# Optimization experiments

Hardware: AMD Instinct MI355X
Metric: run time of the kernel (lower is better)

## Reference

```python
import jax, jax.numpy as jnp
import numpy as np

NUM_GROUPS = 17
NUM_OCCLUDED = 10
TEMP = 0.1


def setup_inputs() -> dict:
    key = jax.random.key(0)
    k1, k2 = jax.random.split(key)
    B, N, D = 128, 577, 768
    x = jax.random.normal(k1, (B, N, D), dtype=jnp.float32)
    # xavier_uniform-like scale for (D, G) weight
    bound = float(np.sqrt(6.0 / (D + NUM_GROUPS)))
    group_weights = jax.random.uniform(k2, (D, NUM_GROUPS), dtype=jnp.float32, minval=-bound, maxval=bound)
    return {"x": x, "group_weights": group_weights}


def _l2_normalize(v):
    # matches F.normalize(dim=-1, eps=1e-12)
    return v / jnp.maximum(jnp.linalg.norm(v, axis=-1, keepdims=True), 1e-12)


def reference(x, group_weights):
    B, N, D = x.shape
    cls_token = x[:, 0, :]            # (B, D)
    patch_tokens = x[:, 1:, :]        # (B, P, D), P = N-1

    # cosine similarity of each patch with cls token
    sim = jnp.einsum('bpd,bd->bp', _l2_normalize(patch_tokens), _l2_normalize(cls_token))  # (B, P)

    # k least-similar patches are "occluded" -> zero them out
    _, occ_idx = jax.lax.top_k(-sim, NUM_OCCLUDED)  # (B, K)
    mask = jnp.ones_like(sim).at[jnp.arange(B)[:, None], occ_idx].set(0.0)  # (B, P)
    non_occ = patch_tokens * mask[..., None]  # (B, P, D)

    # attention-style group pooling; softmax over groups (dim=1)
    scores = jnp.einsum('dg,bpd->bgp', group_weights, non_occ) / TEMP  # (B, G, P)
    attn = jax.nn.softmax(scores, axis=1)
    group_features = jnp.einsum('bgp,bpd->bgd', attn, non_occ)  # (B, G, D)

    # pack [global_feat, group_feat_1..G] as (B, 1+G, D)
    feats = jnp.concatenate([cls_token[:, None, :], group_features], axis=1)
    return feats, attn
```

## Files before the change

kernel.cpp:

```cpp
#include <hip/hip_runtime.h>
#include <math.h>

#define B_ 128
#define NTOK 577
#define P_ 576
#define D_ 768
#define G_ 17
#define KOCC 10
#define INV_TEMP 10.0f
#define U17 (1.0f / 17.0f)
#define NCHUNK 9

#define OFF_WT 0
#define OFF_SIM (G_ * D_)
#define OFF_CLSINV (OFF_SIM + B_ * P_)
#define OFF_GFP (OFF_CLSINV + B_)
#define GFP_PART ((size_t)B_ * G_ * D_)

__global__ __launch_bounds__(256) void k0_cls(const float* __restrict__ x,
                                              const float* __restrict__ gw,
                                              float* __restrict__ feats,
                                              float* __restrict__ clsinv,
                                              float* __restrict__ wt,
                                              int zero_groups) {
    if (blockIdx.x >= B_) {
        int g = blockIdx.x - B_;
        for (int d = threadIdx.x; d < D_; d += 256)
            wt[g * D_ + d] = gw[d * G_ + g];
        return;
    }
    int b = blockIdx.x;
    const float* cls = x + (size_t)b * NTOK * D_;
    float* fb = feats + (size_t)b * 18 * D_;
    float ss = 0.f;
    for (int i = threadIdx.x; i < D_ / 4; i += 256) {
        float4 v = ((const float4*)cls)[i];
        ((float4*)fb)[i] = v;
        ss = fmaf(v.x, v.x, fmaf(v.y, v.y, fmaf(v.z, v.z, fmaf(v.w, v.w, ss))));
    }
    if (zero_groups) {
        float4 z = {0.f, 0.f, 0.f, 0.f};
        for (int i = threadIdx.x; i < G_ * D_ / 4; i += 256)
            ((float4*)(fb + D_))[i] = z;
    }
    #pragma unroll
    for (int off = 32; off; off >>= 1) ss += __shfl_xor(ss, off, 64);
    __shared__ float red[4];
    int wave = threadIdx.x >> 6, lane = threadIdx.x & 63;
    if (lane == 0) red[wave] = ss;
    __syncthreads();
    if (threadIdx.x == 0) {
        float t = red[0] + red[1] + red[2] + red[3];
        clsinv[b] = 1.0f / fmaxf(sqrtf(t), 1e-12f);
    }
}

__global__ __launch_bounds__(256) void k13_score_pv(const float* __restrict__ x,
                                                    const float* __restrict__ wt,
                                                    const float* __restrict__ clsinv,
                                                    float* __restrict__ sim,
                                                    float* __restrict__ attn,
                                                    float* __restrict__ gfp,
                                                    float* __restrict__ feats,
                                                    int use_part) {
    __shared__ __align__(16) float atile[19 * 68];
    int tid = threadIdx.x;
    int b = blockIdx.y, chunk = blockIdx.x;
    const float* clsrow = x + (size_t)b * NTOK * D_;

    int lane = tid & 63, wave = tid >> 6;
    int lr = lane & 15, row4 = lane >> 4;
    int pbase = wave * 16 + row4 * 4;
    const float* xp0 = x + ((size_t)(b * NTOK + 1 + chunk * 64 + pbase)) * D_ + lr * 4;
    const float* wp  = wt + lr * 4;
    const float* cp  = clsrow + lr * 4;

    float4 xv[4], xn[4];
    #pragma unroll
    for (int m = 0; m < 4; ++m) xv[m] = *(const float4*)(xp0 + (size_t)m * D_);
    #pragma unroll
    for (int m = 0; m < 4; ++m) xn[m] = xv[m];

    float s[19][4];
    #pragma unroll
    for (int i = 0; i < 19; ++i)
        #pragma unroll
        for (int m = 0; m < 4; ++m) s[i][m] = 0.f;

    for (int kc = 0; kc < 12; ++kc) {
        if (kc < 11) {
            #pragma unroll
            for (int m = 0; m < 4; ++m)
                xn[m] = *(const float4*)(xp0 + (kc + 1) * 64 + (size_t)m * D_);
        }
        const float* wk = wp + kc * 64;
        float4 cls4 = *(const float4*)(cp + kc * 64);
        #pragma unroll
        for (int g = 0; g < 17; ++g) {
            float4 w4 = *(const float4*)(wk + (size_t)g * D_);
            #pragma unroll
            for (int m = 0; m < 4; ++m)
                s[g][m] = fmaf(xv[m].x, w4.x, fmaf(xv[m].y, w4.y,
                          fmaf(xv[m].z, w4.z, fmaf(xv[m].w, w4.w, s[g][m]))));
        }
        #pragma unroll
        for (int m = 0; m < 4; ++m)
            s[17][m] = fmaf(xv[m].x, cls4.x, fmaf(xv[m].y, cls4.y,
                       fmaf(xv[m].z, cls4.z, fmaf(xv[m].w, cls4.w, s[17][m]))));
        #pragma unroll
        for (int m = 0; m < 4; ++m)
            s[18][m] = fmaf(xv[m].x, xv[m].x, fmaf(xv[m].y, xv[m].y,
                       fmaf(xv[m].z, xv[m].z, fmaf(xv[m].w, xv[m].w, s[18][m]))));
        #pragma unroll
        for (int m = 0; m < 4; ++m) xv[m] = xn[m];
    }

    #pragma unroll
    for (int off = 8; off >= 1; off >>= 1)
        #pragma unroll
        for (int i = 0; i < 19; ++i)
            #pragma unroll
            for (int m = 0; m < 4; ++m)
                s[i][m] += __shfl_xor(s[i][m], off, 16);

    #pragma unroll
    for (int g = 0; g < 19; ++g) {
        if (lr == ((g < 16) ? g : 15)) {
            float4 v = {s[g][0], s[g][1], s[g][2], s[g][3]};
            *(float4*)&atile[g * 68 + pbase] = v;
        }
    }
    __syncthreads();

    if (tid < 64) {
        int p = chunk * 64 + tid;
        float v[17];
        float mx = -3.0e38f;
        #pragma unroll
        for (int g = 0; g < 17; ++g) {
            v[g] = atile[g * 68 + tid];
            mx = fmaxf(mx, v[g]);
        }
        float tot = 0.f;
        #pragma unroll
        for (int g = 0; g < 17; ++g) {
            v[g] = __expf((v[g] - mx) * INV_TEMP);
            tot += v[g];
        }
        float inv = 1.0f / tot;
        float* ap = attn + ((size_t)b * G_) * P_ + p;
        #pragma unroll
        for (int g = 0; g < 17; ++g) {
            float av = v[g] * inv;
            ap[(size_t)g * P_] = av;
            atile[g * 68 + tid] = av;
        }
        float cd = atile[17 * 68 + tid];
        float sq = atile[18 * 68 + tid];
        sim[(size_t)b * P_ + p] = cd * clsinv[b] / fmaxf(sqrtf(sq), 1e-12f);
    }
    __syncthreads();

    if (tid >= 192) return;
    const float* xb = x + ((size_t)(b * NTOK) + 1 + chunk * 64) * D_ + tid * 4;
    float4 acc[G_];
    #pragma unroll
    for (int g = 0; g < G_; ++g) acc[g] = make_float4(0.f, 0.f, 0.f, 0.f);

    float4 c0 = *(const float4*)(xb + (size_t)0 * D_);
    float4 c1 = *(const float4*)(xb + (size_t)1 * D_);
    float4 c2 = *(const float4*)(xb + (size_t)2 * D_);
    float4 c3 = *(const float4*)(xb + (size_t)3 * D_);

    for (int pp = 0; pp < 64; pp += 4) {
        float4 n0 = c0, n1 = c1, n2 = c2, n3 = c3;
        if (pp + 4 < 64) {
            n0 = *(const float4*)(xb + (size_t)(pp + 4) * D_);
            n1 = *(const float4*)(xb + (size_t)(pp + 5) * D_);
            n2 = *(const float4*)(xb + (size_t)(pp + 6) * D_);
            n3 = *(const float4*)(xb + (size_t)(pp + 7) * D_);
        }
        #pragma unroll
        for (int g = 0; g < G_; ++g) {
            float4 a = *(const float4*)&atile[g * 68 + pp];
            acc[g].x = fmaf(a.x, c0.x, fmaf(a.y, c1.x, fmaf(a.z, c2.x, fmaf(a.w, c3.x, acc[g].x))));
            acc[g].y = fmaf(a.x, c0.y, fmaf(a.y, c1.y, fmaf(a.z, c2.y, fmaf(a.w, c3.y, acc[g].y))));
            acc[g].z = fmaf(a.x, c0.z, fmaf(a.y, c1.z, fmaf(a.z, c2.z, fmaf(a.w, c3.z, acc[g].z))));
            acc[g].w = fmaf(a.x, c0.w, fmaf(a.y, c1.w, fmaf(a.z, c2.w, fmaf(a.w, c3.w, acc[g].w))));
        }
        c0 = n0; c1 = n1; c2 = n2; c3 = n3;
    }

    if (use_part) {
        float* gb = gfp + ((size_t)(chunk * B_ + b) * G_) * D_ + tid * 4;
        #pragma unroll
        for (int g = 0; g < G_; ++g) *(float4*)(gb + (size_t)g * D_) = acc[g];
    } else {
        float* fb = feats + ((size_t)(b * 18) + 1) * D_ + tid * 4;
        #pragma unroll
        for (int g = 0; g < G_; ++g) {
            atomicAdd(fb + (size_t)g * D_ + 0, acc[g].x);
            atomicAdd(fb + (size_t)g * D_ + 1, acc[g].y);
            atomicAdd(fb + (size_t)g * D_ + 2, acc[g].z);
            atomicAdd(fb + (size_t)g * D_ + 3, acc[g].w);
        }
    }
}

__global__ __launch_bounds__(192) void k24_fin(const float* __restrict__ x,
                                               const float* __restrict__ sim,
                                               const float* __restrict__ gfp,
                                               float* __restrict__ attn,
                                               float* __restrict__ feats,
                                               int use_part) {
    __shared__ int s_occ[KOCC];
    __shared__ float s_a0[KOCC][G_];
    int b = blockIdx.x, tid = threadIdx.x;

    if (tid < 64) {
        int lane = tid;
        int base = lane * 9;
        float v[9];
        #pragma unroll
        for (int j = 0; j < 9; ++j) v[j] = sim[(size_t)b * P_ + base + j];
        for (int t = 0; t < KOCC; ++t) {
            float mv = 3.0e38f;
            int mi = 1 << 30;
            #pragma unroll
            for (int j = 0; j < 9; ++j) {
                if (v[j] < mv) { mv = v[j]; mi = base + j; }
            }
            #pragma unroll
            for (int off = 1; off < 64; off <<= 1) {
                float ov = __shfl_xor(mv, off, 64);
                int oi = __shfl_xor(mi, off, 64);
                if (ov < mv || (ov == mv && oi < mi)) { mv = ov; mi = oi; }
            }
            if (lane == 0) s_occ[t] = mi;
            int loc = mi - base;
            if (loc >= 0 && loc < 9) v[loc] = 3.0e38f;
        }
    }

    float4 acc[G_];
    float* fb = feats + ((size_t)(b * 18) + 1) * D_ + tid * 4;
    if (use_part) {
        #pragma unroll
        for (int g = 0; g < G_; ++g) acc[g] = make_float4(0.f, 0.f, 0.f, 0.f);
        for (int pc = 0; pc < NCHUNK; ++pc) {
            const float* gb = gfp + ((size_t)(pc * B_ + b) * G_) * D_ + tid * 4;
            #pragma unroll
            for (int g = 0; g < G_; ++g) {
                float4 v = *(const float4*)(gb + (size_t)g * D_);
                acc[g].x += v.x; acc[g].y += v.y; acc[g].z += v.z; acc[g].w += v.w;
            }
        }
    } else {
        #pragma unroll
        for (int g = 0; g < G_; ++g) acc[g] = *(const float4*)(fb + (size_t)g * D_);
    }
    __syncthreads();

    for (int i = tid; i < KOCC * G_; i += 192) {
        int t = i / G_, g = i - t * G_;
        size_t idx = ((size_t)b * G_ + g) * P_ + s_occ[t];
        s_a0[t][g] = attn[idx];
        attn[idx] = U17;
    }
    __syncthreads();

    #pragma unroll
    for (int t = 0; t < KOCC; ++t) {
        float4 xo = *(const float4*)(x + ((size_t)(b * NTOK) + 1 + s_occ[t]) * D_ + tid * 4);
        #pragma unroll
        for (int g = 0; g < G_; ++g) {
            float a0 = s_a0[t][g];
            acc[g].x = fmaf(-a0, xo.x, acc[g].x);
            acc[g].y = fmaf(-a0, xo.y, acc[g].y);
            acc[g].z = fmaf(-a0, xo.z, acc[g].z);
            acc[g].w = fmaf(-a0, xo.w, acc[g].w);
        }
    }
    #pragma unroll
    for (int g = 0; g < G_; ++g) *(float4*)(fb + (size_t)g * D_) = acc[g];
}

extern "C" void kernel_launch(void* const* d_in, const int* in_sizes, int n_in,
                              void* d_out, int out_size, void* d_ws, size_t ws_size,
                              hipStream_t stream) {
    const float* x  = (const float*)d_in[0];
    const float* gw = (const float*)d_in[1];
    float* feats = (float*)d_out;
    float* attn  = (float*)d_out + (size_t)B_ * 18 * D_;
    float* wt      = (float*)d_ws + OFF_WT;
    float* sim     = (float*)d_ws + OFF_SIM;
    float* clsinv  = (float*)d_ws + OFF_CLSINV;
    float* gfp     = (float*)d_ws + OFF_GFP;

    int use_part = (((size_t)OFF_GFP + (size_t)NCHUNK * GFP_PART) * sizeof(float) <= ws_size);

    k0_cls<<<B_ + G_, 256, 0, stream>>>(x, gw, feats, clsinv, wt, !use_part);
    k13_score_pv<<<dim3(NCHUNK, B_), 256, 0, stream>>>(x, wt, clsinv, sim, attn, gfp, feats, use_part);
    k24_fin<<<B_, 192, 0, stream>>>(x, sim, gfp, attn, feats, use_part);
}
```

Measured before the change: 412.8 us.

## Stage group weights in LDS and triple-buffer x loads in score kernel

Copies the whole 17x768 group weight matrix into shared memory at block start, so inner-loop weight reads come from LDS instead of global/L1. It also replaces the double buffer of x rows with a three-slot rotating buffer that prefetches two k-chunks ahead, and reuses the LDS buffer as the score tile after a barrier. The change adds about 52 KB of LDS per block and more live registers, and sets launch_bounds to 3 blocks per CU, which may limit occupancy.

Result: slower. 705.6 us (+70.9%).

```diff
diff --git a/kernel.cpp b/kernel.cpp
--- a/kernel.cpp
+++ b/kernel.cpp
@@ -55,31 +55,42 @@
     }
 }
 
-__global__ __launch_bounds__(256) void k13_score_pv(const float* __restrict__ x,
-                                                    const float* __restrict__ wt,
-                                                    const float* __restrict__ clsinv,
-                                                    float* __restrict__ sim,
-                                                    float* __restrict__ attn,
-                                                    float* __restrict__ gfp,
-                                                    float* __restrict__ feats,
-                                                    int use_part) {
-    __shared__ __align__(16) float atile[19 * 68];
+__global__ __launch_bounds__(256, 3) void k13_score_pv(const float* __restrict__ x,
+                                                       const float* __restrict__ wt,
+                                                       const float* __restrict__ clsinv,
+                                                       float* __restrict__ sim,
+                                                       float* __restrict__ attn,
+                                                       float* __restrict__ gfp,
+                                                       float* __restrict__ feats,
+                                                       int use_part) {
+    __shared__ __align__(16) float wlds[G_ * D_];
+    float* atile = wlds;
+
     int tid = threadIdx.x;
     int b = blockIdx.y, chunk = blockIdx.x;
     const float* clsrow = x + (size_t)b * NTOK * D_;
 
+    for (int i = tid; i < G_ * D_ / 4; i += 256)
+        ((float4*)wlds)[i] = ((const float4*)wt)[i];
+
     int lane = tid & 63, wave = tid >> 6;
     int lr = lane & 15, row4 = lane >> 4;
+    int lr4 = lr * 4;
     int pbase = wave * 16 + row4 * 4;
-    const float* xp0 = x + ((size_t)(b * NTOK + 1 + chunk * 64 + pbase)) * D_ + lr * 4;
-    const float* wp  = wt + lr * 4;
-    const float* cp  = clsrow + lr * 4;
-
-    float4 xv[4], xn[4];
-    #pragma unroll
-    for (int m = 0; m < 4; ++m) xv[m] = *(const float4*)(xp0 + (size_t)m * D_);
-    #pragma unroll
-    for (int m = 0; m < 4; ++m) xn[m] = xv[m];
+    const float* xp0 = x + ((size_t)(b * NTOK + 1 + chunk * 64 + pbase)) * D_ + lr4;
+    const float* cp  = clsrow + lr4;
+
+    float4 xA[4], xB[4], xC[4];
+    float4 cA, cB, cC;
+    #pragma unroll
+    for (int m = 0; m < 4; ++m) xA[m] = *(const float4*)(xp0 + 0 * 64 + (size_t)m * D_);
+    #pragma unroll
+    for (int m = 0; m < 4; ++m) xB[m] = *(const float4*)(xp0 + 1 * 64 + (size_t)m * D_);
+    cA = *(const float4*)(cp + 0 * 64);
+    cB = *(const float4*)(cp + 1 * 64);
+    #pragma unroll
+    for (int m = 0; m < 4; ++m) xC[m] = xA[m];
+    cC = cA;
 
     float s[19][4];
     #pragma unroll
@@ -87,33 +98,42 @@
         #pragma unroll
         for (int m = 0; m < 4; ++m) s[i][m] = 0.f;
 
-    for (int kc = 0; kc < 12; ++kc) {
-        if (kc < 11) {
-            #pragma unroll
-            for (int m = 0; m < 4; ++m)
-                xn[m] = *(const float4*)(xp0 + (kc + 1) * 64 + (size_t)m * D_);
-        }
-        const float* wk = wp + kc * 64;
-        float4 cls4 = *(const float4*)(cp + kc * 64);
-        #pragma unroll
-        for (int g = 0; g < 17; ++g) {
-            float4 w4 = *(const float4*)(wk + (size_t)g * D_);
-            #pragma unroll
-            for (int m = 0; m < 4; ++m)
-                s[g][m] = fmaf(xv[m].x, w4.x, fmaf(xv[m].y, w4.y,
-                          fmaf(xv[m].z, w4.z, fmaf(xv[m].w, w4.w, s[g][m]))));
-        }
-        #pragma unroll
-        for (int m = 0; m < 4; ++m)
-            s[17][m] = fmaf(xv[m].x, cls4.x, fmaf(xv[m].y, cls4.y,
-                       fmaf(xv[m].z, cls4.z, fmaf(xv[m].w, cls4.w, s[17][m]))));
-        #pragma unroll
-        for (int m = 0; m < 4; ++m)
-            s[18][m] = fmaf(xv[m].x, xv[m].x, fmaf(xv[m].y, xv[m].y,
-                       fmaf(xv[m].z, xv[m].z, fmaf(xv[m].w, xv[m].w, s[18][m]))));
-        #pragma unroll
-        for (int m = 0; m < 4; ++m) xv[m] = xn[m];
-    }
+    __syncthreads();
+
+#define SCORE_BODY(XV, CV, XP, CP2, kcur)                                              \
+    do {                                                                               \
+        int kpre = (kcur) + 2;                                                         \
+        if (kpre < 12) {                                                               \
+            _Pragma("unroll")                                                          \
+            for (int m = 0; m < 4; ++m)                                                \
+                XP[m] = *(const float4*)(xp0 + kpre * 64 + (size_t)m * D_);            \
+            CP2 = *(const float4*)(cp + kpre * 64);                                    \
+        }                                                                              \
+        const float* wk = wlds + (kcur) * 64 + lr4;                                    \
+        _Pragma("unroll")                                                              \
+        for (int g = 0; g < 17; ++g) {                                                 \
+            float4 w4 = *(const float4*)(wk + (size_t)g * D_);                         \
+            _Pragma("unroll")                                                          \
+            for (int m = 0; m < 4; ++m)                                                \
+                s[g][m] = fmaf(XV[m].x, w4.x, fmaf(XV[m].y, w4.y,                      \
+                          fmaf(XV[m].z, w4.z, fmaf(XV[m].w, w4.w, s[g][m]))));         \
+        }                                                                              \
+        _Pragma("unroll")                                                              \
+        for (int m = 0; m < 4; ++m)                                                    \
+            s[17][m] = fmaf(XV[m].x, CV.x, fmaf(XV[m].y, CV.y,                         \
+                       fmaf(XV[m].z, CV.z, fmaf(XV[m].w, CV.w, s[17][m]))));           \
+        _Pragma("unroll")                                                              \
+        for (int m = 0; m < 4; ++m)                                                    \
+            s[18][m] = fmaf(XV[m].x, XV[m].x, fmaf(XV[m].y, XV[m].y,                   \
+                       fmaf(XV[m].z, XV[m].z, fmaf(XV[m].w, XV[m].w, s[18][m]))));     \
+    } while (0)
+
+    for (int kc = 0; kc < 12; kc += 3) {
+        SCORE_BODY(xA, cA, xC, cC, kc);
+        SCORE_BODY(xB, cB, xA, cA, kc + 1);
+        SCORE_BODY(xC, cC, xB, cB, kc + 2);
+    }
+#undef SCORE_BODY
 
     #pragma unroll
     for (int off = 8; off >= 1; off >>= 1)
@@ -122,6 +142,8 @@
             #pragma unroll
             for (int m = 0; m < 4; ++m)
                 s[i][m] += __shfl_xor(s[i][m], off, 16);
+
+    __syncthreads();
 
     #pragma unroll
     for (int g = 0; g < 19; ++g) {
```

## Split fused score+PV kernel into separate score and PV kernels

Applied to the files above, without the earlier changes.

Splits the fused scoring/softmax/PV kernel into two kernels. The score kernel runs 512 threads with 2 rows per thread instead of 4, cutting register pressure and raising occupancy. The PV kernel reloads attention from global memory into shared memory. The trade is a second pass over x (about 227MB read again), an extra launch, and a global round trip for attn.

Result: slower. 451.8 us (+9.4%).

```diff
diff --git a/kernel.cpp b/kernel.cpp
--- a/kernel.cpp
+++ b/kernel.cpp
@@ -55,64 +55,57 @@
     }
 }
 
-__global__ __launch_bounds__(256) void k13_score_pv(const float* __restrict__ x,
-                                                    const float* __restrict__ wt,
-                                                    const float* __restrict__ clsinv,
-                                                    float* __restrict__ sim,
-                                                    float* __restrict__ attn,
-                                                    float* __restrict__ gfp,
-                                                    float* __restrict__ feats,
-                                                    int use_part) {
+__global__ __launch_bounds__(512) void k1_score(const float* __restrict__ x,
+                                                const float* __restrict__ wt,
+                                                const float* __restrict__ clsinv,
+                                                float* __restrict__ sim,
+                                                float* __restrict__ attn) {
     __shared__ __align__(16) float atile[19 * 68];
     int tid = threadIdx.x;
     int b = blockIdx.y, chunk = blockIdx.x;
     const float* clsrow = x + (size_t)b * NTOK * D_;
 
     int lane = tid & 63, wave = tid >> 6;
-    int lr = lane & 15, row4 = lane >> 4;
-    int pbase = wave * 16 + row4 * 4;
-    const float* xp0 = x + ((size_t)(b * NTOK + 1 + chunk * 64 + pbase)) * D_ + lr * 4;
-    const float* wp  = wt + lr * 4;
-    const float* cp  = clsrow + lr * 4;
-
-    float4 xv[4], xn[4];
-    #pragma unroll
-    for (int m = 0; m < 4; ++m) xv[m] = *(const float4*)(xp0 + (size_t)m * D_);
-    #pragma unroll
-    for (int m = 0; m < 4; ++m) xn[m] = xv[m];
-
-    float s[19][4];
-    #pragma unroll
-    for (int i = 0; i < 19; ++i)
-        #pragma unroll
-        for (int m = 0; m < 4; ++m) s[i][m] = 0.f;
+    int lr = lane & 15, rh = lane >> 4;
+    int lr4 = lr * 4;
+    int pbase = wave * 8 + rh * 2;
+    const float* xp0 = x + ((size_t)(b * NTOK + 1 + chunk * 64 + pbase)) * D_ + lr4;
+    const float* cp  = clsrow + lr4;
+
+    float4 xv[2], xn[2], cv, cn;
+    xv[0] = *(const float4*)(xp0);
+    xv[1] = *(const float4*)(xp0 + D_);
+    cv = *(const float4*)(cp);
+    xn[0] = xv[0]; xn[1] = xv[1]; cn = cv;
+
+    float s[19][2];
+    #pragma unroll
+    for (int i = 0; i < 19; ++i) { s[i][0] = 0.f; s[i][1] = 0.f; }
 
     for (int kc = 0; kc < 12; ++kc) {
         if (kc < 11) {
-            #pragma unroll
-            for (int m = 0; m < 4; ++m)
-                xn[m] = *(const float4*)(xp0 + (kc + 1) * 64 + (size_t)m * D_);
-        }
-        const float* wk = wp + kc * 64;
-        float4 cls4 = *(const float4*)(cp + kc * 64);
+            xn[0] = *(const float4*)(xp0 + (kc + 1) * 64);
+            xn[1] = *(const float4*)(xp0 + (kc + 1) * 64 + D_);
+            cn = *(const float4*)(cp + (kc + 1) * 64);
+        }
+        const float* wk = wt + kc * 64 + lr4;
         #pragma unroll
         for (int g = 0; g < 17; ++g) {
             float4 w4 = *(const float4*)(wk + (size_t)g * D_);
             #pragma unroll
-            for (int m = 0; m < 4; ++m)
+            for (int m = 0; m < 2; ++m)
                 s[g][m] = fmaf(xv[m].x, w4.x, fmaf(xv[m].y, w4.y,
                           fmaf(xv[m].z, w4.z, fmaf(xv[m].w, w4.w, s[g][m]))));
         }
         #pragma unroll
-        for (int m = 0; m < 4; ++m)
-            s[17][m] = fmaf(xv[m].x, cls4.x, fmaf(xv[m].y, cls4.y,
-                       fmaf(xv[m].z, cls4.z, fmaf(xv[m].w, cls4.w, s[17][m]))));
-        #pragma unroll
-        for (int m = 0; m < 4; ++m)
+        for (int m = 0; m < 2; ++m)
+            s[17][m] = fmaf(xv[m].x, cv.x, fmaf(xv[m].y, cv.y,
+                       fmaf(xv[m].z, cv.z, fmaf(xv[m].w, cv.w, s[17][m]))));
+        #pragma unroll
+        for (int m = 0; m < 2; ++m)
             s[18][m] = fmaf(xv[m].x, xv[m].x, fmaf(xv[m].y, xv[m].y,
                        fmaf(xv[m].z, xv[m].z, fmaf(xv[m].w, xv[m].w, s[18][m]))));
-        #pragma unroll
-        for (int m = 0; m < 4; ++m) xv[m] = xn[m];
+        xv[0] = xn[0]; xv[1] = xn[1]; cv = cn;
     }
 
     #pragma unroll
@@ -120,14 +113,14 @@
         #pragma unroll
         for (int i = 0; i < 19; ++i)
             #pragma unroll
-            for (int m = 0; m < 4; ++m)
+            for (int m = 0; m < 2; ++m)
                 s[i][m] += __shfl_xor(s[i][m], off, 16);
 
     #pragma unroll
     for (int g = 0; g < 19; ++g) {
         if (lr == ((g < 16) ? g : 15)) {
-            float4 v = {s[g][0], s[g][1], s[g][2], s[g][3]};
-            *(float4*)&atile[g * 68 + pbase] = v;
+            float2 v = {s[g][0], s[g][1]};
+            *(float2*)&atile[g * 68 + pbase] = v;
         }
     }
     __syncthreads();
@@ -150,18 +143,28 @@
         float inv = 1.0f / tot;
         float* ap = attn + ((size_t)b * G_) * P_ + p;
         #pragma unroll
-        for (int g = 0; g < 17; ++g) {
-            float av = v[g] * inv;
-            ap[(size_t)g * P_] = av;
-            atile[g * 68 + tid] = av;
-        }
+        for (int g = 0; g < 17; ++g) ap[(size_t)g * P_] = v[g] * inv;
         float cd = atile[17 * 68 + tid];
         float sq = atile[18 * 68 + tid];
         sim[(size_t)b * P_ + p] = cd * clsinv[b] / fmaxf(sqrtf(sq), 1e-12f);
     }
-    __syncthreads();
-
-    if (tid >= 192) return;
+}
+
+__global__ __launch_bounds__(192) void k3_pv(const float* __restrict__ x,
+                                             const float* __restrict__ attn,
+                                             float* __restrict__ gfp,
+                                             float* __restrict__ feats,
+                                             int use_part) {
+    __shared__ __align__(16) float am[17 * 68];
+    int tid = threadIdx.x;
+    int chunk = blockIdx.x, b = blockIdx.y;
+
+    for (int i = tid; i < 17 * 64; i += 192) {
+        int g = i >> 6, p = i & 63;
+        am[g * 68 + p] = attn[((size_t)b * G_ + g) * P_ + chunk * 64 + p];
+    }
+    __syncthreads();
+
     const float* xb = x + ((size_t)(b * NTOK) + 1 + chunk * 64) * D_ + tid * 4;
     float4 acc[G_];
     #pragma unroll
@@ -182,7 +185,7 @@
         }
         #pragma unroll
         for (int g = 0; g < G_; ++g) {
-            float4 a = *(const float4*)&atile[g * 68 + pp];
+            float4 a = *(const float4*)&am[g * 68 + pp];
             acc[g].x = fmaf(a.x, c0.x, fmaf(a.y, c1.x, fmaf(a.z, c2.x, fmaf(a.w, c3.x, acc[g].x))));
             acc[g].y = fmaf(a.x, c0.y, fmaf(a.y, c1.y, fmaf(a.z, c2.y, fmaf(a.w, c3.y, acc[g].y))));
             acc[g].z = fmaf(a.x, c0.z, fmaf(a.y, c1.z, fmaf(a.z, c2.z, fmaf(a.w, c3.z, acc[g].z))));
@@ -300,6 +303,7 @@
     int use_part = (((size_t)OFF_GFP + (size_t)NCHUNK * GFP_PART) * sizeof(float) <= ws_size);
 
     k0_cls<<<B_ + G_, 256, 0, stream>>>(x, gw, feats, clsinv, wt, !use_part);
-    k13_score_pv<<<dim3(NCHUNK, B_), 256, 0, stream>>>(x, wt, clsinv, sim, attn, gfp, feats, use_part);
+    k1_score<<<dim3(NCHUNK, B_), 512, 0, stream>>>(x, wt, clsinv, sim, attn);
+    k3_pv<<<dim3(NCHUNK, B_), 192, 0, stream>>>(x, attn, gfp, feats, use_part);
     k24_fin<<<B_, 192, 0, stream>>>(x, sim, gfp, attn, feats, use_part);
 }
```
